# Kernel optimization log

Measured on AMD Instinct MI355X. Metric: run time of the kernel, lower is better.

Reference implementation:

```python
import jax, jax.numpy as jnp
import numpy as np
import math

N_USER = 100000
N_GAME = 50000
E = 200000
D = 256          # in_dim == out_dim
H = 8            # num_heads
SCALE = math.sqrt(D // H)  # sqrt(head_dim) = sqrt(32)


def setup_inputs() -> dict:
    key = jax.random.key(0)
    keys = jax.random.split(key, 64)
    it = iter(range(64))
    def nk():
        return keys[next(it)]
    s = 1.0 / math.sqrt(D)
    inp = {}
    inp["x_user"] = jax.random.normal(nk(), (N_USER, D), dtype=jnp.float32)
    inp["x_game"] = jax.random.normal(nk(), (N_GAME, D), dtype=jnp.float32)
    # node-type projections (k/q/v/out) for user and game
    for nt in ("user", "game"):
        for p in ("k", "q", "v", "out"):
            inp[f"W{p}_{nt}"] = jax.random.normal(nk(), (D, D), dtype=jnp.float32) * s
            inp[f"b{p}_{nt}"] = jax.random.normal(nk(), (D,), dtype=jnp.float32) * 0.01
    # edge-type attention + message transforms
    for et in ("played", "rev"):
        inp[f"Wa_{et}"] = jax.random.normal(nk(), (D, H), dtype=jnp.float32) * s
        inp[f"ba_{et}"] = jax.random.normal(nk(), (H,), dtype=jnp.float32) * 0.01
        inp[f"Wm_{et}"] = jax.random.normal(nk(), (D, D), dtype=jnp.float32) * s
        inp[f"bm_{et}"] = jax.random.normal(nk(), (D,), dtype=jnp.float32) * 0.01
    # edge indices: played (user -> game), rev_played (game -> user)
    inp["ei_played_src"] = jax.random.randint(nk(), (E,), 0, N_USER, dtype=jnp.int32)
    inp["ei_played_dst"] = jax.random.randint(nk(), (E,), 0, N_GAME, dtype=jnp.int32)
    inp["ei_rev_src"] = jax.random.randint(nk(), (E,), 0, N_GAME, dtype=jnp.int32)
    inp["ei_rev_dst"] = jax.random.randint(nk(), (E,), 0, N_USER, dtype=jnp.int32)
    return inp


def _lin(x, W, b):
    return x @ W + b


def _edge_pass(k_src_all, q_dst_all, v_src_all, Wa, ba, Wm, bm, src, dst, n_dst):
    # gather per-edge K/Q/V                                   [E, D]
    k_src = k_src_all[src]
    q_dst = q_dst_all[dst]
    v_src = v_src_all[src]
    # attention score MLP over head dim                       [E, H]
    scores = ((k_src * q_dst) @ Wa + ba) / SCALE
    attn = jax.nn.softmax(scores, axis=-1)  # softmax over heads (as in source)
    # message MLP                                             [E, D]
    msgs = v_src @ Wm + bm
    weighted = msgs * attn.mean(axis=-1, keepdims=True)
    # scatter-add to destination nodes
    agg = jax.ops.segment_sum(weighted, dst, num_segments=n_dst)
    cnt = jax.ops.segment_sum(jnp.ones((dst.shape[0], 1), weighted.dtype), dst, num_segments=n_dst)
    return agg, cnt


def reference(x_user, x_game,
              Wk_user, bk_user, Wq_user, bq_user, Wv_user, bv_user, Wout_user, bout_user,
              Wk_game, bk_game, Wq_game, bq_game, Wv_game, bv_game, Wout_game, bout_game,
              Wa_played, ba_played, Wm_played, bm_played,
              Wa_rev, ba_rev, Wm_rev, bm_rev,
              ei_played_src, ei_played_dst, ei_rev_src, ei_rev_dst):
    # per-node-type K/Q/V projections
    k_u = _lin(x_user, Wk_user, bk_user)
    q_u = _lin(x_user, Wq_user, bq_user)
    v_u = _lin(x_user, Wv_user, bv_user)
    k_g = _lin(x_game, Wk_game, bk_game)
    q_g = _lin(x_game, Wq_game, bq_game)
    v_g = _lin(x_game, Wv_game, bv_game)

    # user --played--> game
    agg_game, cnt_game = _edge_pass(k_u, q_g, v_u, Wa_played, ba_played, Wm_played, bm_played,
                                    ei_played_src, ei_played_dst, N_GAME)
    # game --rev_played--> user
    agg_user, cnt_user = _edge_pass(k_g, q_u, v_g, Wa_rev, ba_rev, Wm_rev, bm_rev,
                                    ei_rev_src, ei_rev_dst, N_USER)

    def finish(agg, cnt, x, Wout, bout):
        normed = agg / jnp.maximum(cnt, 1.0)
        return jax.nn.relu(_lin(normed, Wout, bout) + x)

    out_user = finish(agg_user, cnt_user, x_user, Wout_user, bout_user)
    out_game = finish(agg_game, cnt_game, x_game, Wout_game, bout_game)
    # concatenate node types for a single output array [N_USER+N_GAME, D]
    return jnp.concatenate([out_user, out_game], axis=0)
```

## Files before the change

### kernel.cpp

```cpp
#include <hip/hip_runtime.h>
#include <cstddef>
#include <cstdint>


#define DD 256
#define SCAN_CHUNK 2048

typedef __attribute__((ext_vector_type(8))) short short8;
typedef __attribute__((ext_vector_type(4))) float floatx4;

__device__ __forceinline__ short f2bf(float f) {
    union { float f; unsigned u; } c;
    c.f = f;
    unsigned r = c.u + 0x7fffu + ((c.u >> 16) & 1u);
    return (short)(r >> 16);
}

__global__ __launch_bounds__(256) void fuseA(const float* __restrict__ A0,
                                             const float* __restrict__ B0,
                                             float* __restrict__ C0,
                                             const float* __restrict__ A1,
                                             const float* __restrict__ B1,
                                             float* __restrict__ C1,
                                             const int* __restrict__ dst0,
                                             int* __restrict__ cnt0, int E0,
                                             const int* __restrict__ dst1,
                                             int* __restrict__ cnt1, int E1) {
    __shared__ float As[DD];
    const int bid = blockIdx.x;
    const int c = threadIdx.x;
    if (bid < 512) {
        const int which = bid >> 8;
        const int r = bid & 255;
        const float* A = which ? A1 : A0;
        const float* B = which ? B1 : B0;
        float* C = which ? C1 : C0;
        As[c] = A[r * DD + c];
        __syncthreads();
        float acc = 0.f;
#pragma unroll 8
        for (int k = 0; k < DD; ++k) acc += As[k] * B[k * DD + c];
        C[r * DD + c] = acc;
    } else {
        const int nb0 = (E0 + 255) >> 8;
        const int b = bid - 512;
        if (b < nb0) {
            const int i = b * 256 + c;
            if (i < E0) atomicAdd(&cnt0[dst0[i]], 1);
        } else {
            const int i = (b - nb0) * 256 + c;
            if (i < E1) atomicAdd(&cnt1[dst1[i]], 1);
        }
    }
}

__global__ __launch_bounds__(256) void fuseB(const float* __restrict__ A0,
                                             const float* __restrict__ B0,
                                             short* __restrict__ C0,
                                             const float* __restrict__ A1,
                                             const float* __restrict__ B1,
                                             short* __restrict__ C1,
                                             int* __restrict__ off_g,
                                             int* __restrict__ sums_g, int n_g,
                                             int* __restrict__ off_u,
                                             int* __restrict__ sums_u, int n_u) {
    __shared__ float As[DD];
    __shared__ int ls[256];
    const int bid = blockIdx.x;
    const int tid = threadIdx.x;
    if (bid < 512) {
        const int which = bid >> 8;
        const int r = bid & 255;
        const int c = tid;
        const float* A = which ? A1 : A0;
        const float* B = which ? B1 : B0;
        short* C = which ? C1 : C0;
        As[c] = A[r * DD + c];
        __syncthreads();
        float acc = 0.f;
#pragma unroll 8
        for (int k = 0; k < DD; ++k) acc += As[k] * B[k * DD + c];
        const int idx = ((((r >> 5) * 16 + (c >> 4)) * 64 +
                          ((c & 15) | (((r >> 3) & 3) << 4))) << 3) + (r & 7);
        C[idx] = f2bf(acc * 0.125f);
    } else {
        const int nch_g = (n_g + SCAN_CHUNK - 1) / SCAN_CHUNK;
        const int b = bid - 512;
        int* off;
        int* sums;
        int n, cb;
        if (b < nch_g) { off = off_g; sums = sums_g; n = n_g; cb = b; }
        else { off = off_u; sums = sums_u; n = n_u; cb = b - nch_g; }
        const int base = cb * SCAN_CHUNK + tid * 8;
        int v[8];
        int s = 0;
#pragma unroll
        for (int i = 0; i < 8; ++i) {
            const int idx = base + i;
            v[i] = (idx < n) ? off[idx] : 0;
            s += v[i];
        }
        ls[tid] = s;
        __syncthreads();
        for (int d = 1; d < 256; d <<= 1) {
            const int t = (tid >= d) ? ls[tid - d] : 0;
            __syncthreads();
            ls[tid] += t;
            __syncthreads();
        }
        int excl = tid ? ls[tid - 1] : 0;
        if (tid == 255) sums[cb] = ls[255];
#pragma unroll
        for (int i = 0; i < 8; ++i) {
            const int idx = base + i;
            if (idx < n) off[idx] = excl;
            excl += v[i];
        }
    }
}

__global__ __launch_bounds__(256) void fuseC(const float* __restrict__ bv0,
                                             const float* __restrict__ Wm0,
                                             const float* __restrict__ bm0,
                                             const float* __restrict__ Wout0,
                                             float* __restrict__ bb0,
                                             const float* __restrict__ bv1,
                                             const float* __restrict__ Wm1,
                                             const float* __restrict__ bm1,
                                             const float* __restrict__ Wout1,
                                             float* __restrict__ bb1,
                                             int* __restrict__ sums_g, int nch_g,
                                             int* __restrict__ sums_u, int nch_u) {
    __shared__ float t[DD];
    __shared__ int ls[256];
    const int tid = threadIdx.x;
    if (blockIdx.x < 2) {
        const int w = blockIdx.x;
        const float* bv = w ? bv1 : bv0;
        const float* Wm = w ? Wm1 : Wm0;
        const float* bm = w ? bm1 : bm0;
        const float* Wout = w ? Wout1 : Wout0;
        float* bb = w ? bb1 : bb0;
        float acc = bm[tid];
#pragma unroll 8
        for (int k = 0; k < DD; ++k) acc += bv[k] * Wm[k * DD + tid];
        t[tid] = acc;
        __syncthreads();
        float acc2 = 0.f;
#pragma unroll 8
        for (int k = 0; k < DD; ++k) acc2 += t[k] * Wout[k * DD + tid];
        bb[tid] = acc2 * 0.125f;
    } else {
        int* sums = (blockIdx.x == 2) ? sums_g : sums_u;
        const int nch = (blockIdx.x == 2) ? nch_g : nch_u;
        ls[tid] = (tid < nch) ? sums[tid] : 0;
        __syncthreads();
        for (int d = 1; d < 256; d <<= 1) {
            const int t2 = (tid >= d) ? ls[tid - d] : 0;
            __syncthreads();
            ls[tid] += t2;
            __syncthreads();
        }
        if (tid < nch) sums[tid] = tid ? ls[tid - 1] : 0;
    }
}

__global__ __launch_bounds__(256) void fuseD(int* __restrict__ off_g,
                                             const int* __restrict__ sums_g,
                                             int* __restrict__ cur_g, int n_g, int Eg,
                                             int* __restrict__ off_u,
                                             const int* __restrict__ sums_u,
                                             int* __restrict__ cur_u, int n_u, int Eu) {
    const int gidx = blockIdx.x * 256 + threadIdx.x;
    const int span_g = n_g + 1;
    if (gidx < span_g) {
        if (gidx < n_g) {
            const int v = off_g[gidx] + sums_g[gidx / SCAN_CHUNK];
            off_g[gidx] = v;
            cur_g[gidx] = v;
        } else {
            off_g[n_g] = Eg;
        }
    } else {
        const int idx = gidx - span_g;
        if (idx < n_u) {
            const int v = off_u[idx] + sums_u[idx / SCAN_CHUNK];
            off_u[idx] = v;
            cur_u[idx] = v;
        } else if (idx == n_u) {
            off_u[n_u] = Eu;
        }
    }
}

__global__ __launch_bounds__(256) void fuseE(const int* __restrict__ src0,
                                             const int* __restrict__ dst0,
                                             int* __restrict__ cur0,
                                             int* __restrict__ perm0, int E0,
                                             const int* __restrict__ src1,
                                             const int* __restrict__ dst1,
                                             int* __restrict__ cur1,
                                             int* __restrict__ perm1, int E1) {
    const int nb0 = (E0 + 255) >> 8;
    const int b = blockIdx.x;
    const int tid = threadIdx.x;
    if (b < nb0) {
        const int i = b * 256 + tid;
        if (i < E0) {
            const int pos = atomicAdd(&cur0[dst0[i]], 1);
            perm0[pos] = src0[i];
        }
    } else {
        const int i = (b - nb0) * 256 + tid;
        if (i < E1) {
            const int pos = atomicAdd(&cur1[dst1[i]], 1);
            perm1[pos] = src1[i];
        }
    }
}

__global__ __launch_bounds__(256, 4) void agg_gemm5(
    const float* __restrict__ x_user, const float* __restrict__ x_game,
    const int* __restrict__ perm_rev, const int* __restrict__ off_user,
    const short* __restrict__ Bsw_rev, const float* __restrict__ bb_rev,
    const float* __restrict__ bout_user,
    const int* __restrict__ perm_played, const int* __restrict__ off_game,
    const short* __restrict__ Bsw_played, const float* __restrict__ bb_played,
    const float* __restrict__ bout_game,
    float* __restrict__ outp, int n_user, int n_game, int nb_game) {
    __shared__ short As[32][264];
    __shared__ float bt[32];

    const int tid = threadIdx.x;
    const int wave = __builtin_amdgcn_readfirstlane(tid >> 6);
    const int lane = tid & 63;

    const float* x_src;
    const float* x_res;
    const int* perm;
    const int* off;
    const short* Bsw;
    const float* bb;
    const float* bout;
    float* out;
    int M, r0;
    if ((int)blockIdx.x < nb_game) {
        x_src = x_user; x_res = x_game;
        perm = perm_played; off = off_game;
        Bsw = Bsw_played; bb = bb_played; bout = bout_game;
        out = outp + (size_t)n_user * DD;
        M = n_game;
        r0 = (int)blockIdx.x * 32;
    } else {
        x_src = x_game; x_res = x_user;
        perm = perm_rev; off = off_user;
        Bsw = Bsw_rev; bb = bb_rev; bout = bout_user;
        out = outp;
        M = n_user;
        r0 = ((int)blockIdx.x - nb_game) * 32;
    }

    int eb[8], deg[8];
    int s0[8], s1[8];
    float4 acc[8];
#pragma unroll
    for (int j = 0; j < 8; ++j) {
        const int r = r0 + wave * 8 + j;
        eb[j] = (r < M) ? off[r] : 0;
        const int e1 = (r < M) ? off[r + 1] : 0;
        deg[j] = e1 - eb[j];
        acc[j].x = 0.f; acc[j].y = 0.f; acc[j].z = 0.f; acc[j].w = 0.f;
        if (lane == 0) bt[wave * 8 + j] = (deg[j] > 0) ? 1.0f : 0.0f;
    }
#pragma unroll
    for (int j = 0; j < 8; ++j) {
        s0[j] = (deg[j] > 0) ? perm[eb[j]] : 0;
        s1[j] = (deg[j] > 1) ? perm[eb[j] + 1] : 0;
    }
    int mdeg = 0;
#pragma unroll
    for (int j = 0; j < 8; ++j) mdeg = max(mdeg, deg[j]);

    for (int t = 0; t < mdeg; ++t) {
        float4 v[8];
        bool h[8];
#pragma unroll
        for (int j = 0; j < 8; ++j) {
            h[j] = t < deg[j];
            if (h[j])
                v[j] = ((const float4*)(x_src + (size_t)s0[j] * DD))[lane];
        }
        int s2[8];
#pragma unroll
        for (int j = 0; j < 8; ++j)
            s2[j] = (t + 2 < deg[j]) ? perm[eb[j] + t + 2] : 0;
#pragma unroll
        for (int j = 0; j < 8; ++j) {
            if (h[j]) {
                acc[j].x += v[j].x;
                acc[j].y += v[j].y;
                acc[j].z += v[j].z;
                acc[j].w += v[j].w;
            }
            s0[j] = s1[j];
            s1[j] = s2[j];
        }
    }
#pragma unroll
    for (int j = 0; j < 8; ++j) {
        const int lr = wave * 8 + j;
        const float inv = 1.0f / fmaxf((float)deg[j], 1.0f);
        short4 b4;
        b4.x = f2bf(acc[j].x * inv);
        b4.y = f2bf(acc[j].y * inv);
        b4.z = f2bf(acc[j].z * inv);
        b4.w = f2bf(acc[j].w * inv);
        *(short4*)&As[lr][lane * 4] = b4;
    }
    __syncthreads();

    const int quad = lane >> 4;
    const int l16 = lane & 15;
    floatx4 cacc[2][4];
#pragma unroll
    for (int rt = 0; rt < 2; ++rt)
#pragma unroll
        for (int ct = 0; ct < 4; ++ct) cacc[rt][ct] = (floatx4){0.f, 0.f, 0.f, 0.f};

    for (int kb8 = 0; kb8 < 8; ++kb8) {
        short8 af[2];
#pragma unroll
        for (int rt = 0; rt < 2; ++rt)
            af[rt] = *(const short8*)&As[rt * 16 + l16][kb8 * 32 + quad * 8];
        short8 bf[4];
        const short* bp = Bsw + (((size_t)(kb8 * 16 + wave * 4) * 64 + lane) << 3);
#pragma unroll
        for (int ct = 0; ct < 4; ++ct)
            bf[ct] = *(const short8*)(bp + (ct << 9));
#pragma unroll
        for (int rt = 0; rt < 2; ++rt)
#pragma unroll
            for (int ct = 0; ct < 4; ++ct)
                cacc[rt][ct] = __builtin_amdgcn_mfma_f32_16x16x32_bf16(
                    af[rt], bf[ct], cacc[rt][ct], 0, 0, 0);
    }

    float bbv[4], bov[4];
#pragma unroll
    for (int ct = 0; ct < 4; ++ct) {
        const int n = wave * 64 + ct * 16 + l16;
        bbv[ct] = bb[n];
        bov[ct] = bout[n];
    }
#pragma unroll
    for (int rt = 0; rt < 2; ++rt) {
#pragma unroll
        for (int j = 0; j < 4; ++j) {
            const int lr = rt * 16 + quad * 4 + j;
            const int r = r0 + lr;
            if (r < M) {
                const float btv = bt[lr];
                const float* xr = x_res + (size_t)r * DD;
                float* orow = out + (size_t)r * DD;
#pragma unroll
                for (int ct = 0; ct < 4; ++ct) {
                    const int n = wave * 64 + ct * 16 + l16;
                    const float o = cacc[rt][ct][j] + btv * bbv[ct] + bov[ct] + xr[n];
                    orow[n] = fmaxf(o, 0.f);
                }
            }
        }
    }
}

extern "C" void kernel_launch(void* const* d_in, const int* in_sizes, int n_in,
                              void* d_out, int out_size, void* d_ws, size_t ws_size,
                              hipStream_t stream) {
    const float* x_user = (const float*)d_in[0];
    const float* x_game = (const float*)d_in[1];
    const float* Wv_user = (const float*)d_in[6];
    const float* bv_user = (const float*)d_in[7];
    const float* Wout_user = (const float*)d_in[8];
    const float* bout_user = (const float*)d_in[9];
    const float* Wv_game = (const float*)d_in[14];
    const float* bv_game = (const float*)d_in[15];
    const float* Wout_game = (const float*)d_in[16];
    const float* bout_game = (const float*)d_in[17];
    const float* Wm_played = (const float*)d_in[20];
    const float* bm_played = (const float*)d_in[21];
    const float* Wm_rev = (const float*)d_in[24];
    const float* bm_rev = (const float*)d_in[25];
    const int* ei_played_src = (const int*)d_in[26];
    const int* ei_played_dst = (const int*)d_in[27];
    const int* ei_rev_src = (const int*)d_in[28];
    const int* ei_rev_dst = (const int*)d_in[29];

    const int n_user = in_sizes[0] / DD;
    const int n_game = in_sizes[1] / DD;
    const int e_played = in_sizes[26];
    const int e_rev = in_sizes[28];

    float* out = (float*)d_out;
    float* out_user = out;
    float* out_game = out + (size_t)n_user * DD;
    (void)out_game; (void)out_user;

    float* fws = (float*)d_ws;
    float* T0 = fws;
    float* T1 = T0 + DD * DD;
    float* bb_played = T1 + DD * DD;
    float* bb_rev = bb_played + DD;
    short* Bsw_played = (short*)(bb_rev + DD);
    short* Bsw_rev = Bsw_played + DD * DD;
    int* iws = (int*)(Bsw_rev + DD * DD);
    int* off_game = iws;
    int* off_user = off_game + (n_game + 1);
    int* cursor_game = off_user + (n_user + 1);
    int* cursor_user = cursor_game + n_game;
    int* sums_game = cursor_user + n_user;
    int* sums_user = sums_game + 256;
    int* perm_played = sums_user + 256;
    int* perm_rev = perm_played + e_played;
    (void)ws_size; (void)n_in; (void)out_size;

    hipMemsetAsync(off_game, 0, (size_t)(n_game + n_user + 2) * sizeof(int), stream);

    const int nbh_p = (e_played + 255) / 256;
    const int nbh_r = (e_rev + 255) / 256;
    const int nch_g = (n_game + SCAN_CHUNK - 1) / SCAN_CHUNK;
    const int nch_u = (n_user + SCAN_CHUNK - 1) / SCAN_CHUNK;

    fuseA<<<512 + nbh_p + nbh_r, 256, 0, stream>>>(
        Wv_user, Wm_played, T0, Wv_game, Wm_rev, T1,
        ei_played_dst, off_game, e_played, ei_rev_dst, off_user, e_rev);
    fuseB<<<512 + nch_g + nch_u, 256, 0, stream>>>(
        T0, Wout_game, Bsw_played, T1, Wout_user, Bsw_rev,
        off_game, sums_game, n_game, off_user, sums_user, n_user);
    fuseC<<<4, 256, 0, stream>>>(
        bv_user, Wm_played, bm_played, Wout_game, bb_played,
        bv_game, Wm_rev, bm_rev, Wout_user, bb_rev,
        sums_game, nch_g, sums_user, nch_u);
    const int ntot = (n_game + 1) + (n_user + 1);
    fuseD<<<(ntot + 255) / 256, 256, 0, stream>>>(
        off_game, sums_game, cursor_game, n_game, e_played,
        off_user, sums_user, cursor_user, n_user, e_rev);
    fuseE<<<nbh_p + nbh_r, 256, 0, stream>>>(
        ei_played_src, ei_played_dst, cursor_game, perm_played, e_played,
        ei_rev_src, ei_rev_dst, cursor_user, perm_rev, e_rev);

    const int nb_game = (n_game + 31) / 32;
    const int nb_user = (n_user + 31) / 32;
    agg_gemm5<<<nb_game + nb_user, 256, 0, stream>>>(
        x_user, x_game, perm_rev, off_user, Bsw_rev, bb_rev, bout_user,
        perm_played, off_game, Bsw_played, bb_played, bout_game,
        out, n_user, n_game, nb_game);
}
```

Before: 469.9 us.

## Pre-convert node features to bf16 for halved gather traffic in aggregation

Adds a conversion pass, run inside the fuseE scatter kernel, that writes x_user and x_game as bf16 into workspace. The aggregation kernel then gathers bf16 rows, half the bytes of the fp32 rows, and sums them in fp32. The residual read and output write now use nontemporal hints. The conversion costs a full extra read of both inputs plus a bf16 write, and the aggregated means lose some precision to bf16 rounding.

```diff
diff --git a/kernel.cpp b/kernel.cpp
--- a/kernel.cpp
+++ b/kernel.cpp
@@ -5,15 +5,27 @@
 
 #define DD 256
 #define SCAN_CHUNK 2048
+#define NCONV 2048
 
 typedef __attribute__((ext_vector_type(8))) short short8;
 typedef __attribute__((ext_vector_type(4))) float floatx4;
+typedef __attribute__((ext_vector_type(4))) short shortx4;
 
 __device__ __forceinline__ short f2bf(float f) {
     union { float f; unsigned u; } c;
     c.f = f;
     unsigned r = c.u + 0x7fffu + ((c.u >> 16) & 1u);
     return (short)(r >> 16);
+}
+__device__ __forceinline__ float bflo(unsigned u) {
+    union { unsigned u; float f; } c;
+    c.u = u << 16;
+    return c.f;
+}
+__device__ __forceinline__ float bfhi(unsigned u) {
+    union { unsigned u; float f; } c;
+    c.u = u & 0xffff0000u;
+    return c.f;
 }
 
 __global__ __launch_bounds__(256) void fuseA(const float* __restrict__ A0,
@@ -200,8 +212,14 @@
                                              const int* __restrict__ src1,
                                              const int* __restrict__ dst1,
                                              int* __restrict__ cur1,
-                                             int* __restrict__ perm1, int E1) {
+                                             int* __restrict__ perm1, int E1,
+                                             const float* __restrict__ xu,
+                                             const float* __restrict__ xg,
+                                             short* __restrict__ xbf,
+                                             int n_user, int n_game) {
     const int nb0 = (E0 + 255) >> 8;
+    const int nb1 = (E1 + 255) >> 8;
+    const int nbperm = nb0 + nb1;
     const int b = blockIdx.x;
     const int tid = threadIdx.x;
     if (b < nb0) {
@@ -210,16 +228,34 @@
             const int pos = atomicAdd(&cur0[dst0[i]], 1);
             perm0[pos] = src0[i];
         }
-    } else {
+    } else if (b < nbperm) {
         const int i = (b - nb0) * 256 + tid;
         if (i < E1) {
             const int pos = atomicAdd(&cur1[dst1[i]], 1);
             perm1[pos] = src1[i];
         }
-    }
-}
-
-__global__ __launch_bounds__(256, 4) void agg_gemm5(
+    } else {
+        const size_t u4 = (size_t)n_user * 64;
+        const size_t tot4 = u4 + (size_t)n_game * 64;
+        const size_t stride = (size_t)NCONV * 256;
+        for (size_t i = (size_t)(b - nbperm) * 256 + tid; i < tot4; i += stride) {
+            floatx4 v;
+            if (i < u4)
+                v = __builtin_nontemporal_load((const floatx4*)xu + i);
+            else
+                v = __builtin_nontemporal_load((const floatx4*)xg + (i - u4));
+            shortx4 b4;
+            b4.x = f2bf(v.x);
+            b4.y = f2bf(v.y);
+            b4.z = f2bf(v.z);
+            b4.w = f2bf(v.w);
+            *((shortx4*)xbf + i) = b4;
+        }
+    }
+}
+
+__global__ __launch_bounds__(256, 4) void agg_gemm6(
+    const short* __restrict__ xbf,
     const float* __restrict__ x_user, const float* __restrict__ x_game,
     const int* __restrict__ perm_rev, const int* __restrict__ off_user,
     const short* __restrict__ Bsw_rev, const float* __restrict__ bb_rev,
@@ -235,7 +271,7 @@
     const int wave = __builtin_amdgcn_readfirstlane(tid >> 6);
     const int lane = tid & 63;
 
-    const float* x_src;
+    const short* xb_src;
     const float* x_res;
     const int* perm;
     const int* off;
@@ -245,14 +281,16 @@
     float* out;
     int M, r0;
     if ((int)blockIdx.x < nb_game) {
-        x_src = x_user; x_res = x_game;
+        xb_src = xbf;
+        x_res = x_game;
         perm = perm_played; off = off_game;
         Bsw = Bsw_played; bb = bb_played; bout = bout_game;
         out = outp + (size_t)n_user * DD;
         M = n_game;
         r0 = (int)blockIdx.x * 32;
     } else {
-        x_src = x_game; x_res = x_user;
+        xb_src = xbf + (size_t)n_user * DD;
+        x_res = x_user;
         perm = perm_rev; off = off_user;
         Bsw = Bsw_rev; bb = bb_rev; bout = bout_user;
         out = outp;
@@ -282,13 +320,13 @@
     for (int j = 0; j < 8; ++j) mdeg = max(mdeg, deg[j]);
 
     for (int t = 0; t < mdeg; ++t) {
-        float4 v[8];
+        uint2 d[8];
         bool h[8];
 #pragma unroll
         for (int j = 0; j < 8; ++j) {
             h[j] = t < deg[j];
             if (h[j])
-                v[j] = ((const float4*)(x_src + (size_t)s0[j] * DD))[lane];
+                d[j] = *((const uint2*)(xb_src + (size_t)s0[j] * DD) + lane);
         }
         int s2[8];
 #pragma unroll
@@ -297,10 +335,10 @@
 #pragma unroll
         for (int j = 0; j < 8; ++j) {
             if (h[j]) {
-                acc[j].x += v[j].x;
-                acc[j].y += v[j].y;
-                acc[j].z += v[j].z;
-                acc[j].w += v[j].w;
+                acc[j].x += bflo(d[j].x);
+                acc[j].y += bfhi(d[j].x);
+                acc[j].z += bflo(d[j].y);
+                acc[j].w += bfhi(d[j].y);
             }
             s0[j] = s1[j];
             s1[j] = s2[j];
@@ -365,8 +403,9 @@
 #pragma unroll
                 for (int ct = 0; ct < 4; ++ct) {
                     const int n = wave * 64 + ct * 16 + l16;
-                    const float o = cacc[rt][ct][j] + btv * bbv[ct] + bov[ct] + xr[n];
-                    orow[n] = fmaxf(o, 0.f);
+                    const float xv = __builtin_nontemporal_load(xr + n);
+                    const float o = cacc[rt][ct][j] + btv * bbv[ct] + bov[ct] + xv;
+                    __builtin_nontemporal_store(fmaxf(o, 0.f), orow + n);
                 }
             }
         }
@@ -401,9 +440,6 @@
     const int e_rev = in_sizes[28];
 
     float* out = (float*)d_out;
-    float* out_user = out;
-    float* out_game = out + (size_t)n_user * DD;
-    (void)out_game; (void)out_user;
 
     float* fws = (float*)d_ws;
     float* T0 = fws;
@@ -421,6 +457,9 @@
     int* sums_user = sums_game + 256;
     int* perm_played = sums_user + 256;
     int* perm_rev = perm_played + e_played;
+    uintptr_t xaddr = (uintptr_t)(perm_rev + e_rev);
+    xaddr = (xaddr + 255) & ~(uintptr_t)255;
+    short* xbf = (short*)xaddr;
     (void)ws_size; (void)n_in; (void)out_size;
 
     hipMemsetAsync(off_game, 0, (size_t)(n_game + n_user + 2) * sizeof(int), stream);
@@ -444,14 +483,15 @@
     fuseD<<<(ntot + 255) / 256, 256, 0, stream>>>(
         off_game, sums_game, cursor_game, n_game, e_played,
         off_user, sums_user, cursor_user, n_user, e_rev);
-    fuseE<<<nbh_p + nbh_r, 256, 0, stream>>>(
+    fuseE<<<nbh_p + nbh_r + NCONV, 256, 0, stream>>>(
         ei_played_src, ei_played_dst, cursor_game, perm_played, e_played,
-        ei_rev_src, ei_rev_dst, cursor_user, perm_rev, e_rev);
+        ei_rev_src, ei_rev_dst, cursor_user, perm_rev, e_rev,
+        x_user, x_game, xbf, n_user, n_game);
 
     const int nb_game = (n_game + 31) / 32;
     const int nb_user = (n_user + 31) / 32;
-    agg_gemm5<<<nb_game + nb_user, 256, 0, stream>>>(
-        x_user, x_game, perm_rev, off_user, Bsw_rev, bb_rev, bout_user,
+    agg_gemm6<<<nb_game + nb_user, 256, 0, stream>>>(
+        xbf, x_user, x_game, perm_rev, off_user, Bsw_rev, bb_rev, bout_user,
         perm_played, off_game, Bsw_played, bb_played, bout_game,
         out, n_user, n_game, nb_game);
 }
```

Result: slower. 498.7 us (+6.1%).
